# Optimization experiments

Hardware: AMD Instinct MI355X
Metric: run time of the kernel (lower is better)

Reference implementation:

```python
import jax, jax.numpy as jnp
import numpy as np

B, C, N, K = 8, 192, 3136, 9
COUT = 384


def setup_inputs() -> dict:
    key = jax.random.key(0)
    k1, k2, k3, k4 = jax.random.split(key, 4)
    x = jax.random.normal(k1, (B, C, N, 1), dtype=jnp.float32)
    edge_index = jax.random.randint(k2, (2, B, N, K), 0, N, dtype=jnp.int64)
    # 1x1 conv params: BasicConv([2C, COUT]) with bias, act='relu'
    W = jax.random.normal(k3, (COUT, 2 * C), dtype=jnp.float32) * (1.0 / np.sqrt(2 * C))
    b = jax.random.normal(k4, (COUT,), dtype=jnp.float32) * 0.01
    return {"x": x, "edge_index": edge_index, "W": W, "b": b}


def _gather(xs, idx):
    # xs: [B, C, N]; idx: [B, N, K] -> [B, C, N, K]
    return jax.vmap(lambda xb, ib: xb[:, ib])(xs, idx)


def reference(x, edge_index, W, b):
    xs = x[..., 0]                       # [B, C, N]
    x_i = _gather(xs, edge_index[1])     # [B, C, N, K] center features
    x_j = _gather(xs, edge_index[0])     # [B, C, N, K] neighbor features
    feat = jnp.concatenate([x_i, x_j - x_i], axis=1)  # [B, 2C, N, K]
    # 1x1 conv + bias + relu
    h = jnp.einsum('oi,bink->bonk', W, feat) + b[None, :, None, None]
    h = jax.nn.relu(h)                   # [B, COUT, N, K]
    return jnp.max(h, axis=-1, keepdims=True)  # [B, COUT, N, 1]
```

## Files before the change

### kernel.cpp

```cpp
#include <hip/hip_runtime.h>
#include <hip/hip_bf16.h>


#define Bb   8
#define Cc   192
#define Nn   3136
#define Kk   9
#define CO   384
#define TWOC 384
#define JTOT 768
#define PADC 200

typedef short  short8 __attribute__((ext_vector_type(8)));
typedef float  f32x4  __attribute__((ext_vector_type(4)));

__device__ __forceinline__ float bf2f(unsigned int u16) {
    union { unsigned int i; float f; } c;
    c.i = u16 << 16;
    return c.f;
}
__device__ __forceinline__ short f2bf(float f) {
    __hip_bfloat16 h = __float2bfloat16(f);
    short s; __builtin_memcpy(&s, &h, 2); return s;
}

__global__ __launch_bounds__(256) void prep_fused(const void* __restrict__ x_,
                                                  const void* __restrict__ W_,
                                                  const int* __restrict__ ei,
                                                  short* __restrict__ xT,
                                                  short* __restrict__ A_Tb,
                                                  int* __restrict__ flags) {
    __shared__ float s[64][33];
    __shared__ int sflag;
    const int tid = threadIdx.x;
    const int bid = blockIdx.x;

    if (tid < 64) {
        unsigned int u = ((const unsigned short*)x_)[2 * tid];
        int bige = (((u >> 7) & 0xFFu) >= 0x88u);
        unsigned long long bf = __ballot(bige);
        int f32 = (bf != 0ull) ? 1 : 0;
        if (tid == 0) sflag = f32;
        if (bid == 0) {
            int oddnz = (ei[2 * tid + 1] != 0);
            unsigned long long bo = __ballot(oddnz);
            if (tid == 0) {
                flags[0] = f32;
                flags[1] = (bo == 0ull) ? 1 : 0;
            }
        }
    }
    __syncthreads();
    const int fp32 = sflag;

    if (bid < 2352) {
        int b   = bid / 294;
        int rem = bid - b * 294;
        int ct  = rem / 49;
        int nt  = rem - ct * 49;
        const int n0 = nt * 64;
        const int c0 = ct * 32;
        const int cl   = tid >> 3;
        const int nseg = tid & 7;

        if (fp32) {
            const float* p = (const float*)x_ + ((size_t)b * Cc + c0 + cl) * Nn + n0 + nseg * 8;
            float4 v0 = *(const float4*)p;
            float4 v1 = *(const float4*)(p + 4);
            int nb = nseg * 8;
            s[nb + 0][cl] = v0.x;  s[nb + 1][cl] = v0.y;
            s[nb + 2][cl] = v0.z;  s[nb + 3][cl] = v0.w;
            s[nb + 4][cl] = v1.x;  s[nb + 5][cl] = v1.y;
            s[nb + 6][cl] = v1.z;  s[nb + 7][cl] = v1.w;
        } else {
            const unsigned short* p = (const unsigned short*)x_ + ((size_t)b * Cc + c0 + cl) * Nn + n0 + nseg * 8;
            ushort4 u0 = *(const ushort4*)p;
            ushort4 u1 = *(const ushort4*)(p + 4);
            int nb = nseg * 8;
            s[nb + 0][cl] = bf2f(u0.x);  s[nb + 1][cl] = bf2f(u0.y);
            s[nb + 2][cl] = bf2f(u0.z);  s[nb + 3][cl] = bf2f(u0.w);
            s[nb + 4][cl] = bf2f(u1.x);  s[nb + 5][cl] = bf2f(u1.y);
            s[nb + 6][cl] = bf2f(u1.z);  s[nb + 7][cl] = bf2f(u1.w);
        }
        __syncthreads();

        const int nl = tid >> 2;
        const int cs = tid & 3;
        short8 o;
#pragma unroll
        for (int i = 0; i < 8; ++i) o[i] = f2bf(s[nl][cs * 8 + i]);
        *(short8*)(xT + ((size_t)b * Nn + n0 + nl) * PADC + c0 + cs * 8) = o;
    } else {
        int t = (bid - 2352) * 256 + tid;
        int j = t / Cc;
        int c = t - j * Cc;
        int row = (j < CO) ? j : (j - CO);
        float w1, w2;
        if (fp32) {
            const float* W = (const float*)W_;
            w1 = W[row * TWOC + c];  w2 = W[row * TWOC + Cc + c];
        } else {
            const unsigned short* W = (const unsigned short*)W_;
            w1 = bf2f(W[row * TWOC + c]);  w2 = bf2f(W[row * TWOC + Cc + c]);
        }
        A_Tb[(size_t)j * PADC + c] = f2bf((j < CO) ? (w1 - w2) : w2);
    }
}

#define MT 64
#define NT 256
#define KT 32
#define LPAD 40

__global__ __launch_bounds__(256) void gemm_mfma(const short* __restrict__ xT,
                                                 const short* __restrict__ A_Tb,
                                                 short* __restrict__ T) {
    __shared__ short Asl[MT * LPAD];
    __shared__ short Bsl[NT * LPAD];

    const int n0 = blockIdx.x * MT;
    const int j0 = blockIdx.y * NT;
    const int b  = blockIdx.z;
    const int tid  = threadIdx.x;
    const int w    = tid >> 6;
    const int lane = tid & 63;
    const int col  = lane & 15;
    const int quad = lane >> 4;

    f32x4 acc[4][4];
#pragma unroll
    for (int i = 0; i < 4; ++i)
#pragma unroll
        for (int jf = 0; jf < 4; ++jf) acc[i][jf] = (f32x4)(0.0f);

    const int ar = tid >> 2;
    const int ag = tid & 3;

    for (int c0 = 0; c0 < Cc; c0 += KT) {
        *(short8*)(Asl + ar * LPAD + ag * 8) =
            *(const short8*)(xT + ((size_t)b * Nn + n0 + ar) * PADC + c0 + ag * 8);
#pragma unroll
        for (int h = 0; h < 4; ++h) {
            int row = h * 64 + ar;
            *(short8*)(Bsl + row * LPAD + ag * 8) =
                *(const short8*)(A_Tb + (size_t)(j0 + row) * PADC + c0 + ag * 8);
        }
        __syncthreads();

        short8 bf[4];
#pragma unroll
        for (int jf = 0; jf < 4; ++jf)
            bf[jf] = *(const short8*)(&Bsl[(w * 64 + jf * 16 + col) * LPAD + quad * 8]);
#pragma unroll
        for (int fm = 0; fm < 4; ++fm) {
            short8 a = *(const short8*)(&Asl[(fm * 16 + col) * LPAD + quad * 8]);
#pragma unroll
            for (int jf = 0; jf < 4; ++jf)
                acc[fm][jf] = __builtin_amdgcn_mfma_f32_16x16x32_bf16(a, bf[jf], acc[fm][jf], 0, 0, 0);
        }
        __syncthreads();
    }

    const int jbase = j0 + w * 64;
#pragma unroll
    for (int fn = 0; fn < 4; ++fn) {
        int j = jbase + fn * 16 + col;
#pragma unroll
        for (int fm = 0; fm < 4; ++fm) {
#pragma unroll
            for (int r = 0; r < 4; ++r) {
                int n = n0 + fm * 16 + quad * 4 + r;
                T[((size_t)(b * Nn + n)) * JTOT + j] = f2bf(acc[fm][fn][r]);
            }
        }
    }
}

__global__ __launch_bounds__(384) void gather_max(const int* __restrict__ ei,
                                                  const short* __restrict__ T,
                                                  const void* __restrict__ bias_,
                                                  void* __restrict__ out_,
                                                  const int* __restrict__ flags) {
    __shared__ float sm[32][193];
    __shared__ int si0[32][Kk];
    __shared__ int si1[32][Kk];

    const int fp32 = flags[0];
    const int is64 = flags[1];
    const int bid  = blockIdx.x;
    const int b    = bid & 7;
    const int rest = bid >> 3;
    const int half = rest / 98;
    const int n0   = (rest % 98) * 32;
    const int tid  = threadIdx.x;

    for (int s = tid; s < 32 * 2 * Kk; s += 384) {
        int ln = s / (2 * Kk);
        int slot = s - ln * (2 * Kk);
        int n = n0 + ln;
        size_t pos; int* dstp;
        if (slot < Kk) { pos = ((size_t)b * Nn + n) * Kk + slot;               dstp = &si0[ln][slot]; }
        else           { pos = ((size_t)(Bb + b) * Nn + n) * Kk + (slot - Kk); dstp = &si1[ln][slot - Kk]; }
        int v = is64 ? ei[2 * pos] : ei[pos];
        *dstp = (v < 0) ? 0 : (v >= Nn ? Nn - 1 : v);
    }
    __syncthreads();

    const int p   = tid % 96;
    const int seg = tid / 96;
    const int och = half * 192 + 2 * p;
    const unsigned short* Tb = (const unsigned short*)T + (size_t)b * Nn * JTOT;

    float b0, b1;
    if (fp32) {
        b0 = ((const float*)bias_)[och];
        b1 = ((const float*)bias_)[och + 1];
    } else {
        b0 = bf2f(((const unsigned short*)bias_)[och]);
        b1 = bf2f(((const unsigned short*)bias_)[och + 1]);
    }

    for (int ln = seg * 8; ln < seg * 8 + 8; ++ln) {
        float m0 = -INFINITY, m1 = -INFINITY;
#pragma unroll
        for (int k = 0; k < Kk; ++k) {
            unsigned int uu = *(const unsigned int*)(Tb + (size_t)si1[ln][k] * JTOT + och);
            unsigned int vv = *(const unsigned int*)(Tb + (size_t)si0[ln][k] * JTOT + CO + och);
            m0 = fmaxf(m0, bf2f(uu & 0xffffu) + bf2f(vv & 0xffffu));
            m1 = fmaxf(m1, bf2f(uu >> 16) + bf2f(vv >> 16));
        }
        sm[ln][2 * p]     = fmaxf(m0 + b0, 0.0f);
        sm[ln][2 * p + 1] = fmaxf(m1 + b1, 0.0f);
    }
    __syncthreads();

    const int g = tid >> 5, l = tid & 31;
    if (fp32) {
        float* op = (float*)out_;
#pragma unroll
        for (int rr = 0; rr < 16; ++rr) {
            int ol = g * 16 + rr;
            int o  = half * 192 + ol;
            op[((size_t)b * CO + o) * Nn + n0 + l] = sm[l][ol];
        }
    } else {
        __hip_bfloat16* op = (__hip_bfloat16*)out_;
#pragma unroll
        for (int rr = 0; rr < 16; ++rr) {
            int ol = g * 16 + rr;
            int o  = half * 192 + ol;
            op[((size_t)b * CO + o) * Nn + n0 + l] = __float2bfloat16(sm[l][ol]);
        }
    }
}

extern "C" void kernel_launch(void* const* d_in, const int* in_sizes, int n_in,
                              void* d_out, int out_size, void* d_ws, size_t ws_size,
                              hipStream_t stream) {
    const void* x  = d_in[0];
    const int*  ei = (const int*)d_in[1];
    const void* W  = d_in[2];
    const void* bs = d_in[3];

    char* ws = (char*)d_ws;
    int*   flags = (int*)ws;
    short* A_Tb  = (short*)(ws + 1024);
    short* xT    = (short*)(ws + (512u << 10));
    short* T     = (short*)(ws + (11u << 20));

    prep_fused<<<2352 + 576, 256, 0, stream>>>(x, W, ei, xT, A_Tb, flags);

    dim3 g1(Nn / MT, JTOT / NT, Bb);
    gemm_mfma<<<g1, 256, 0, stream>>>(xT, A_Tb, T);

    gather_max<<<Bb * 2 * (Nn / 32), 384, 0, stream>>>(ei, T, bs, d_out, flags);
}
```

Baseline: 146.2 us.

## Split gather_max into channel quarters with 8-byte loads and nontemporal stores

The gather-max kernel now splits output channels into four quarters instead of two, which doubles the grid. Each thread handles 4 channels for 2 nodes using 8-byte loads instead of 2 channels for 8 nodes with 4-byte loads. Stores of xT, the GEMM output T and the final output now use nontemporal hints. The aim is more parallelism and wider loads in the gather, at the cost of loading the index tables twice as often. The nontemporal hint on T may hurt, because the gather kernel reads T right afterwards and would benefit from it staying in cache.

```diff
diff --git a/kernel.cpp b/kernel.cpp
--- a/kernel.cpp
+++ b/kernel.cpp
@@ -89,7 +89,7 @@
         short8 o;
 #pragma unroll
         for (int i = 0; i < 8; ++i) o[i] = f2bf(s[nl][cs * 8 + i]);
-        *(short8*)(xT + ((size_t)b * Nn + n0 + nl) * PADC + c0 + cs * 8) = o;
+        __builtin_nontemporal_store(o, (short8*)(xT + ((size_t)b * Nn + n0 + nl) * PADC + c0 + cs * 8));
     } else {
         int t = (bid - 2352) * 256 + tid;
         int j = t / Cc;
@@ -170,7 +170,8 @@
 #pragma unroll
             for (int r = 0; r < 4; ++r) {
                 int n = n0 + fm * 16 + quad * 4 + r;
-                T[((size_t)(b * Nn + n)) * JTOT + j] = f2bf(acc[fm][fn][r]);
+                __builtin_nontemporal_store(f2bf(acc[fm][fn][r]),
+                                            T + ((size_t)(b * Nn + n)) * JTOT + j);
             }
         }
     }
@@ -181,7 +182,7 @@
                                                   const void* __restrict__ bias_,
                                                   void* __restrict__ out_,
                                                   const int* __restrict__ flags) {
-    __shared__ float sm[32][193];
+    __shared__ float sm[32][97];
     __shared__ int si0[32][Kk];
     __shared__ int si1[32][Kk];
 
@@ -190,7 +191,7 @@
     const int bid  = blockIdx.x;
     const int b    = bid & 7;
     const int rest = bid >> 3;
-    const int half = rest / 98;
+    const int quarter = rest / 98;
     const int n0   = (rest % 98) * 32;
     const int tid  = threadIdx.x;
 
@@ -206,31 +207,36 @@
     }
     __syncthreads();
 
-    const int p   = tid % 96;
-    const int seg = tid / 96;
-    const int och = half * 192 + 2 * p;
+    const int cg  = tid % 24;
+    const int seg = tid / 24;
+    const int och = quarter * 96 + cg * 4;
     const unsigned short* Tb = (const unsigned short*)T + (size_t)b * Nn * JTOT;
 
-    float b0, b1;
+    float b0, b1, b2, b3;
     if (fp32) {
-        b0 = ((const float*)bias_)[och];
-        b1 = ((const float*)bias_)[och + 1];
+        const float* bp = (const float*)bias_ + och;
+        b0 = bp[0]; b1 = bp[1]; b2 = bp[2]; b3 = bp[3];
     } else {
-        b0 = bf2f(((const unsigned short*)bias_)[och]);
-        b1 = bf2f(((const unsigned short*)bias_)[och + 1]);
-    }
-
-    for (int ln = seg * 8; ln < seg * 8 + 8; ++ln) {
-        float m0 = -INFINITY, m1 = -INFINITY;
+        const unsigned short* bp = (const unsigned short*)bias_ + och;
+        b0 = bf2f(bp[0]); b1 = bf2f(bp[1]); b2 = bf2f(bp[2]); b3 = bf2f(bp[3]);
+    }
+
+#pragma unroll
+    for (int t = 0; t < 2; ++t) {
+        int ln = seg * 2 + t;
+        float m0 = -INFINITY, m1 = -INFINITY, m2 = -INFINITY, m3 = -INFINITY;
 #pragma unroll
         for (int k = 0; k < Kk; ++k) {
-            unsigned int uu = *(const unsigned int*)(Tb + (size_t)si1[ln][k] * JTOT + och);
-            unsigned int vv = *(const unsigned int*)(Tb + (size_t)si0[ln][k] * JTOT + CO + och);
-            m0 = fmaxf(m0, bf2f(uu & 0xffffu) + bf2f(vv & 0xffffu));
-            m1 = fmaxf(m1, bf2f(uu >> 16) + bf2f(vv >> 16));
-        }
-        sm[ln][2 * p]     = fmaxf(m0 + b0, 0.0f);
-        sm[ln][2 * p + 1] = fmaxf(m1 + b1, 0.0f);
+            uint2 uu = *(const uint2*)(Tb + (size_t)si1[ln][k] * JTOT + och);
+            uint2 vv = *(const uint2*)(Tb + (size_t)si0[ln][k] * JTOT + CO + och);
+            m0 = fmaxf(m0, bf2f(uu.x & 0xffffu) + bf2f(vv.x & 0xffffu));
+            m1 = fmaxf(m1, bf2f(uu.x >> 16)     + bf2f(vv.x >> 16));
+            m2 = fmaxf(m2, bf2f(uu.y & 0xffffu) + bf2f(vv.y & 0xffffu));
+            m3 = fmaxf(m3, bf2f(uu.y >> 16)     + bf2f(vv.y >> 16));
+        }
+        float4 r = make_float4(fmaxf(m0 + b0, 0.0f), fmaxf(m1 + b1, 0.0f),
+                               fmaxf(m2 + b2, 0.0f), fmaxf(m3 + b3, 0.0f));
+        *(float4*)&sm[ln][cg * 4] = r;
     }
     __syncthreads();
 
@@ -238,18 +244,19 @@
     if (fp32) {
         float* op = (float*)out_;
 #pragma unroll
-        for (int rr = 0; rr < 16; ++rr) {
-            int ol = g * 16 + rr;
-            int o  = half * 192 + ol;
-            op[((size_t)b * CO + o) * Nn + n0 + l] = sm[l][ol];
+        for (int rr = 0; rr < 8; ++rr) {
+            int ol = g * 8 + rr;
+            int o  = quarter * 96 + ol;
+            __builtin_nontemporal_store(sm[l][ol], op + ((size_t)b * CO + o) * Nn + n0 + l);
         }
     } else {
-        __hip_bfloat16* op = (__hip_bfloat16*)out_;
-#pragma unroll
-        for (int rr = 0; rr < 16; ++rr) {
-            int ol = g * 16 + rr;
-            int o  = half * 192 + ol;
-            op[((size_t)b * CO + o) * Nn + n0 + l] = __float2bfloat16(sm[l][ol]);
+        unsigned short* op = (unsigned short*)out_;
+#pragma unroll
+        for (int rr = 0; rr < 8; ++rr) {
+            int ol = g * 8 + rr;
+            int o  = quarter * 96 + ol;
+            __builtin_nontemporal_store((unsigned short)f2bf(sm[l][ol]),
+                                        op + ((size_t)b * CO + o) * Nn + n0 + l);
         }
     }
 }
@@ -273,5 +280,5 @@
     dim3 g1(Nn / MT, JTOT / NT, Bb);
     gemm_mfma<<<g1, 256, 0, stream>>>(xT, A_Tb, T);
 
-    gather_max<<<Bb * 2 * (Nn / 32), 384, 0, stream>>>(ei, T, bs, d_out, flags);
-}
+    gather_max<<<Bb * 4 * (Nn / 32), 384, 0, stream>>>(ei, T, bs, d_out, flags);
+}
```

Result: slower. 169.7 us (+16.0%).

## Retile GEMM to 64x64 full-K blocks with LDS-staged coalesced stores; widen gather loads

Applied to the files above, without the earlier changes.

The GEMM moves from 64x256 tiles with a K-loop of 32 to 64x64 tiles that load the whole K=192 slice into LDS once. Results are staged through LDS and written as 16-byte vector rows instead of scattered 2-byte stores. This gives more blocks for occupancy and coalesced output writes, but less reuse of each loaded tile. The gather-max kernel now has each thread handle 4 channels with 8-byte loads instead of 2 channels with 4-byte loads, cutting the number of load instructions.

```diff
diff --git a/kernel.cpp b/kernel.cpp
--- a/kernel.cpp
+++ b/kernel.cpp
@@ -107,19 +107,14 @@
     }
 }
 
-#define MT 64
-#define NT 256
-#define KT 32
-#define LPAD 40
-
 __global__ __launch_bounds__(256) void gemm_mfma(const short* __restrict__ xT,
                                                  const short* __restrict__ A_Tb,
                                                  short* __restrict__ T) {
-    __shared__ short Asl[MT * LPAD];
-    __shared__ short Bsl[NT * LPAD];
-
-    const int n0 = blockIdx.x * MT;
-    const int j0 = blockIdx.y * NT;
+    __shared__ short Asl[64 * PADC];
+    __shared__ short Bsl[64 * PADC];
+
+    const int n0 = blockIdx.x * 64;
+    const int j0 = blockIdx.y * 64;
     const int b  = blockIdx.z;
     const int tid  = threadIdx.x;
     const int w    = tid >> 6;
@@ -127,51 +122,51 @@
     const int col  = lane & 15;
     const int quad = lane >> 4;
 
-    f32x4 acc[4][4];
-#pragma unroll
-    for (int i = 0; i < 4; ++i)
-#pragma unroll
-        for (int jf = 0; jf < 4; ++jf) acc[i][jf] = (f32x4)(0.0f);
-
-    const int ar = tid >> 2;
-    const int ag = tid & 3;
-
-    for (int c0 = 0; c0 < Cc; c0 += KT) {
-        *(short8*)(Asl + ar * LPAD + ag * 8) =
-            *(const short8*)(xT + ((size_t)b * Nn + n0 + ar) * PADC + c0 + ag * 8);
-#pragma unroll
-        for (int h = 0; h < 4; ++h) {
-            int row = h * 64 + ar;
-            *(short8*)(Bsl + row * LPAD + ag * 8) =
-                *(const short8*)(A_Tb + (size_t)(j0 + row) * PADC + c0 + ag * 8);
-        }
-        __syncthreads();
-
-        short8 bf[4];
-#pragma unroll
-        for (int jf = 0; jf < 4; ++jf)
-            bf[jf] = *(const short8*)(&Bsl[(w * 64 + jf * 16 + col) * LPAD + quad * 8]);
+#pragma unroll
+    for (int i = 0; i < 6; ++i) {
+        int g   = tid + i * 256;
+        int row = g / 24;
+        int pos = g - row * 24;
+        *(short8*)(Asl + row * PADC + pos * 8) =
+            *(const short8*)(xT + ((size_t)b * Nn + n0 + row) * PADC + pos * 8);
+        *(short8*)(Bsl + row * PADC + pos * 8) =
+            *(const short8*)(A_Tb + (size_t)(j0 + row) * PADC + pos * 8);
+    }
+    __syncthreads();
+
+    f32x4 acc[4];
+#pragma unroll
+    for (int i = 0; i < 4; ++i) acc[i] = (f32x4)(0.0f);
+
+#pragma unroll
+    for (int kf = 0; kf < 6; ++kf) {
+        short8 bfr = *(const short8*)(Bsl + (w * 16 + col) * PADC + kf * 32 + quad * 8);
 #pragma unroll
         for (int fm = 0; fm < 4; ++fm) {
-            short8 a = *(const short8*)(&Asl[(fm * 16 + col) * LPAD + quad * 8]);
-#pragma unroll
-            for (int jf = 0; jf < 4; ++jf)
-                acc[fm][jf] = __builtin_amdgcn_mfma_f32_16x16x32_bf16(a, bf[jf], acc[fm][jf], 0, 0, 0);
-        }
-        __syncthreads();
-    }
-
-    const int jbase = j0 + w * 64;
-#pragma unroll
-    for (int fn = 0; fn < 4; ++fn) {
-        int j = jbase + fn * 16 + col;
-#pragma unroll
-        for (int fm = 0; fm < 4; ++fm) {
-#pragma unroll
-            for (int r = 0; r < 4; ++r) {
-                int n = n0 + fm * 16 + quad * 4 + r;
-                T[((size_t)(b * Nn + n)) * JTOT + j] = f2bf(acc[fm][fn][r]);
-            }
+            short8 a = *(const short8*)(Asl + (fm * 16 + col) * PADC + kf * 32 + quad * 8);
+            acc[fm] = __builtin_amdgcn_mfma_f32_16x16x32_bf16(a, bfr, acc[fm], 0, 0, 0);
+        }
+    }
+    __syncthreads();
+
+    short* Ct = Asl;
+#pragma unroll
+    for (int fm = 0; fm < 4; ++fm) {
+#pragma unroll
+        for (int r = 0; r < 4; ++r) {
+            Ct[(fm * 16 + quad * 4 + r) * 72 + w * 16 + col] = f2bf(acc[fm][r]);
+        }
+    }
+    __syncthreads();
+
+    {
+        const int row = tid >> 2;
+        const int gq  = tid & 3;
+#pragma unroll
+        for (int i = 0; i < 2; ++i) {
+            int g = gq + i * 4;
+            *(short8*)(T + ((size_t)(b * Nn + n0 + row)) * JTOT + j0 + g * 8) =
+                *(const short8*)(Ct + row * 72 + g * 8);
         }
     }
 }
@@ -206,31 +201,37 @@
     }
     __syncthreads();
 
-    const int p   = tid % 96;
-    const int seg = tid / 96;
-    const int och = half * 192 + 2 * p;
+    const int cg  = tid % 48;
+    const int seg = tid / 48;
+    const int och = half * 192 + cg * 4;
     const unsigned short* Tb = (const unsigned short*)T + (size_t)b * Nn * JTOT;
 
-    float b0, b1;
+    float b0, b1, b2, b3;
     if (fp32) {
-        b0 = ((const float*)bias_)[och];
-        b1 = ((const float*)bias_)[och + 1];
+        const float* bp = (const float*)bias_ + och;
+        b0 = bp[0]; b1 = bp[1]; b2 = bp[2]; b3 = bp[3];
     } else {
-        b0 = bf2f(((const unsigned short*)bias_)[och]);
-        b1 = bf2f(((const unsigned short*)bias_)[och + 1]);
-    }
-
-    for (int ln = seg * 8; ln < seg * 8 + 8; ++ln) {
-        float m0 = -INFINITY, m1 = -INFINITY;
+        const unsigned short* bp = (const unsigned short*)bias_ + och;
+        b0 = bf2f(bp[0]); b1 = bf2f(bp[1]); b2 = bf2f(bp[2]); b3 = bf2f(bp[3]);
+    }
+
+#pragma unroll
+    for (int t = 0; t < 4; ++t) {
+        int ln = seg * 4 + t;
+        float m0 = -INFINITY, m1 = -INFINITY, m2 = -INFINITY, m3 = -INFINITY;
 #pragma unroll
         for (int k = 0; k < Kk; ++k) {
-            unsigned int uu = *(const unsigned int*)(Tb + (size_t)si1[ln][k] * JTOT + och);
-            unsigned int vv = *(const unsigned int*)(Tb + (size_t)si0[ln][k] * JTOT + CO + och);
-            m0 = fmaxf(m0, bf2f(uu & 0xffffu) + bf2f(vv & 0xffffu));
-            m1 = fmaxf(m1, bf2f(uu >> 16) + bf2f(vv >> 16));
-        }
-        sm[ln][2 * p]     = fmaxf(m0 + b0, 0.0f);
-        sm[ln][2 * p + 1] = fmaxf(m1 + b1, 0.0f);
+            uint2 uu = *(const uint2*)(Tb + (size_t)si1[ln][k] * JTOT + och);
+            uint2 vv = *(const uint2*)(Tb + (size_t)si0[ln][k] * JTOT + CO + och);
+            m0 = fmaxf(m0, bf2f(uu.x & 0xffffu) + bf2f(vv.x & 0xffffu));
+            m1 = fmaxf(m1, bf2f(uu.x >> 16)     + bf2f(vv.x >> 16));
+            m2 = fmaxf(m2, bf2f(uu.y & 0xffffu) + bf2f(vv.y & 0xffffu));
+            m3 = fmaxf(m3, bf2f(uu.y >> 16)     + bf2f(vv.y >> 16));
+        }
+        sm[ln][cg * 4 + 0] = fmaxf(m0 + b0, 0.0f);
+        sm[ln][cg * 4 + 1] = fmaxf(m1 + b1, 0.0f);
+        sm[ln][cg * 4 + 2] = fmaxf(m2 + b2, 0.0f);
+        sm[ln][cg * 4 + 3] = fmaxf(m3 + b3, 0.0f);
     }
     __syncthreads();
 
@@ -270,7 +271,7 @@
 
     prep_fused<<<2352 + 576, 256, 0, stream>>>(x, W, ei, xT, A_Tb, flags);
 
-    dim3 g1(Nn / MT, JTOT / NT, Bb);
+    dim3 g1(Nn / 64, JTOT / 64, Bb);
     gemm_mfma<<<g1, 256, 0, stream>>>(xT, A_Tb, T);
 
     gather_max<<<Bb * 2 * (Nn / 32), 384, 0, stream>>>(ei, T, bs, d_out, flags);
```

Measured after the change: 133.3 us. 8.9% less time.
